# Performance work log

Hardware: AMD Instinct MI355X
Metric: run time of the kernel (lower is better)

## Reference

```python
import jax, jax.numpy as jnp
import numpy as np

DEPTH = 16      # env_depth: number of sequential beam-search steps
TEMP = 20.0     # softmax temperature (forward default temp=20)
NEG = -1e9      # -inf surrogate for dead beams (grad-safe)


def setup_inputs() -> dict:
    key = jax.random.key(0)
    ks = jax.random.split(key, 7)
    B, H, D = 256, 512, 64
    u = lambda k, s: jax.random.uniform(k, s, jnp.float32, -0.1, 0.1)
    return {
        "env": jax.random.normal(ks[0], (B, D), jnp.float32),
        "root_state": u(ks[1], (1, H)),
        "W_logits": u(ks[2], (H, D)),
        "b_logits": u(ks[3], (D,)),
        "W_hh": u(ks[4], (H, H)),
        "b_hh": u(ks[5], (H,)),
        "emb": u(ks[6], (D, H)),
        "beams": 128,
    }


def reference(env, root_state, W_logits, b_logits, W_hh, b_hh, emb, beams):
    B = env.shape[0]
    H = root_state.shape[1]
    D = W_logits.shape[1]

    # All beams start at the (shared, learned) root state; only beam 0 is live.
    states = jnp.broadcast_to(root_state[None, :, :], (B, beams, H))  # [B, K, H]
    scores = jnp.where(jnp.arange(beams) == 0, 0.0, NEG).astype(jnp.float32)
    scores = jnp.broadcast_to(scores[None, :], (B, beams))            # [B, K]
    hist = jnp.zeros((B, beams, DEPTH), jnp.int32)                    # chosen decisions

    def step(carry, t):
        states, scores, hist = carry
        # RNN router step: logits over decisions, temperature-scaled log-softmax
        logits = jnp.einsum('bkh,hd->bkd', states, W_logits) + b_logits  # [B,K,D]
        logp = jax.nn.log_softmax(logits / TEMP, axis=-1)
        # cumulative beam scores over all beams*decisions candidates
        cand = (scores[..., None] + logp).reshape(B, beams * D)
        top_scores, top_idx = jax.lax.top_k(cand, beams)                 # [B,K]
        beam_idx = top_idx // D                                          # parent beam
        dec = top_idx % D                                                # chosen decision
        # gather surviving beam state + history
        sel = jnp.take_along_axis(states, beam_idx[..., None], axis=1)   # [B,K,H]
        hist = jnp.take_along_axis(hist, beam_idx[..., None], axis=1)
        hist = hist.at[:, :, t].set(dec)
        # recurrent state update conditioned on chosen decision
        new_states = jnp.tanh(jnp.einsum('bkh,hg->bkg', sel, W_hh) + b_hh + emb[dec])
        return (new_states, top_scores, hist), None

    (states, scores, hist), _ = jax.lax.scan(step, (states, scores, hist), jnp.arange(DEPTH))
    return hist, scores
```

## Files before the change

### kernel.cpp

```cpp
#include <hip/hip_runtime.h>
#include <hip/hip_bf16.h>
#include <math.h>

#define NB    256
#define NK    128
#define NH    512
#define ND    64
#define NDEPTH 16
#define BKROWS (NB*NK)
#define TEMPD 20.0

typedef double d4 __attribute__((ext_vector_type(4)));

__global__ void k_init(const float* __restrict__ root, float* __restrict__ states,
                       double* __restrict__ scores, unsigned char* __restrict__ hist) {
    int idx = blockIdx.x * 256 + threadIdx.x;
    states[idx] = root[idx & (NH - 1)];
    if (idx < BKROWS) scores[idx] = ((idx & (NK - 1)) == 0) ? 0.0 : -1e9;
    if (idx < BKROWS * NDEPTH) hist[idx] = 0;
}

__global__ void __launch_bounds__(256, 4)
k_logits(const float* __restrict__ states,
         const float* __restrict__ Wl,
         const float* __restrict__ bl,
         const double* __restrict__ scores,
         double* __restrict__ cand)
{
    __shared__ double wl[16][64];
    __shared__ double stT[16][67];
    const int rowb = blockIdx.x * 64;
    const int t    = threadIdx.x;
    const int lane = t & 63;
    const int wv   = t >> 6;
    const int li   = lane & 15;
    const int kq   = lane >> 4;

    d4 acc[4];
    #pragma unroll
    for (int c = 0; c < 4; ++c) { acc[c][0]=0.0; acc[c][1]=0.0; acc[c][2]=0.0; acc[c][3]=0.0; }

    for (int kc = 0; kc < NH; kc += 16) {
        #pragma unroll
        for (int j = 0; j < 2; ++j) {
            int idx = j * 256 + t;
            int row = idx >> 5, cp = idx & 31;
            float2 v = *(const float2*)&Wl[(size_t)(kc + row) * ND + 2 * cp];
            double2 d; d.x = (double)v.x; d.y = (double)v.y;
            *(double2*)&wl[row][2 * cp] = d;
        }
        #pragma unroll
        for (int j = 0; j < 2; ++j) {
            int idx = j * 256 + t;
            int r = idx >> 3, cp = idx & 7;
            float2 v = *(const float2*)&states[(size_t)(rowb + r) * NH + kc + 2 * cp];
            stT[2 * cp][r]     = (double)v.x;
            stT[2 * cp + 1][r] = (double)v.y;
        }
        __syncthreads();

        #pragma unroll
        for (int ks = 0; ks < 4; ++ks) {
            int kk = 4 * ks + kq;
            double a  = stT[kk][wv * 16 + li];
            double b0 = wl[kk][     li];
            double b1 = wl[kk][16 + li];
            double b2 = wl[kk][32 + li];
            double b3 = wl[kk][48 + li];
            acc[0] = __builtin_amdgcn_mfma_f64_16x16x4f64(a, b0, acc[0], 0, 0, 0);
            acc[1] = __builtin_amdgcn_mfma_f64_16x16x4f64(a, b1, acc[1], 0, 0, 0);
            acc[2] = __builtin_amdgcn_mfma_f64_16x16x4f64(a, b2, acc[2], 0, 0, 0);
            acc[3] = __builtin_amdgcn_mfma_f64_16x16x4f64(a, b3, acc[3], 0, 0, 0);
        }
        __syncthreads();
    }

    const double bd0 = (double)bl[li];
    const double bd1 = (double)bl[16 + li];
    const double bd2 = (double)bl[32 + li];
    const double bd3 = (double)bl[48 + li];
    #pragma unroll
    for (int n = 0; n < 4; ++n) {
        int row = rowb + wv * 16 + kq + 4 * n;
        double x0 = (acc[0][n] + bd0) / TEMPD;
        double x1 = (acc[1][n] + bd1) / TEMPD;
        double x2 = (acc[2][n] + bd2) / TEMPD;
        double x3 = (acc[3][n] + bd3) / TEMPD;
        double m = fmax(fmax(x0, x1), fmax(x2, x3));
        #pragma unroll
        for (int off = 1; off <= 8; off <<= 1) m = fmax(m, __shfl_xor(m, off, 64));
        double e = exp(x0 - m) + exp(x1 - m) + exp(x2 - m) + exp(x3 - m);
        #pragma unroll
        for (int off = 1; off <= 8; off <<= 1) e += __shfl_xor(e, off, 64);
        double ls = log(e);
        double sc = scores[row];
        cand[(size_t)row * ND +      li] = sc + x0 - m - ls;
        cand[(size_t)row * ND + 16 + li] = sc + x1 - m - ls;
        cand[(size_t)row * ND + 32 + li] = sc + x2 - m - ls;
        cand[(size_t)row * ND + 48 + li] = sc + x3 - m - ls;
    }
}

__global__ void __launch_bounds__(256)
k_topk(const double* __restrict__ cand,
       double* __restrict__ scores,
       int* __restrict__ parent, int* __restrict__ decs,
       const unsigned char* __restrict__ hist_in,
       unsigned char* __restrict__ hist_out,
       int tstep)
{
    extern __shared__ double smem[];
    double* L  = smem;
    int*    sp = (int*)(smem + 128 * 65);
    int*    sd = sp + NK;

    const int b = blockIdx.x;
    const int t = threadIdx.x;
    const double* cb = cand + (size_t)b * (NK * ND);

    #pragma unroll
    for (int j = 0; j < 32; ++j) {
        int i = j * 256 + t;
        L[(i >> 6) * 65 + (i & 63)] = cb[i];
    }
    __syncthreads();

    if (t < 64) {
        const int lane = t;
        double mv = L[lane]; int mi = lane;
        for (int i = 1; i < 128; ++i) {
            double v = L[i * 65 + lane];
            if (v > mv) { mv = v; mi = i * 64 + lane; }
        }
        for (int it = 0; it < NK; ++it) {
            double m = mv; int idx = mi;
            #pragma unroll
            for (int off = 1; off <= 32; off <<= 1) {
                double m2 = __shfl_xor(m, off, 64);
                int    i2 = __shfl_xor(idx, off, 64);
                if (m2 > m || (m2 == m && i2 < idx)) { m = m2; idx = i2; }
            }
            const int wrow = idx >> 6, wcol = idx & 63;
            if (lane == 0) {
                scores[b * NK + it] = m;
                parent[b * NK + it] = wrow;
                decs  [b * NK + it] = wcol;
                sp[it] = wrow; sd[it] = wcol;
            }
            if (lane == wcol) L[wrow * 65 + wcol] = -INFINITY;
            double r0 = L[(2 * lane) * 65 + wcol];
            double r1 = L[(2 * lane + 1) * 65 + wcol];
            double rm; int ri;
            if (r1 > r0) { rm = r1; ri = (2 * lane + 1) * 64 + wcol; }
            else         { rm = r0; ri = (2 * lane) * 64 + wcol; }
            #pragma unroll
            for (int off = 1; off <= 32; off <<= 1) {
                double m2 = __shfl_xor(rm, off, 64);
                int    i2 = __shfl_xor(ri, off, 64);
                if (m2 > rm || (m2 == rm && i2 < ri)) { rm = m2; ri = i2; }
            }
            if (lane == wcol) { mv = rm; mi = ri; }
        }
    }
    __syncthreads();

    for (int i = t; i < NK * NDEPTH; i += 256) {
        int k = i >> 4, j = i & 15;
        hist_out[(b * NK + k) * NDEPTH + j] = (j == tstep) ? (unsigned char)sd[k]
                                            : hist_in[(b * NK + sp[k]) * NDEPTH + j];
    }
}

__global__ void __launch_bounds__(256, 4)
k_rnn(const float* __restrict__ states_in,
      const float* __restrict__ Whh,
      const float* __restrict__ bhh,
      const float* __restrict__ emb,
      const int* __restrict__ parent, const int* __restrict__ decs,
      float* __restrict__ states_out)
{
    __shared__ double wt[16][128];
    __shared__ double stT[16][67];
    __shared__ int sp[64], sd[64];

    const int rowb = blockIdx.x * 64;
    const int cbk  = blockIdx.y;
    const int colb = cbk * 128;
    const int t    = threadIdx.x;
    const int lane = t & 63;
    const int li   = lane & 15;
    const int kq   = lane >> 4;
    const int wv   = t >> 6;
    const int wm   = wv >> 1;
    const int wn   = wv & 1;

    if (t < 64) { sp[t] = parent[rowb + t]; sd[t] = decs[rowb + t]; }
    __syncthreads();

    int srow[2];
    #pragma unroll
    for (int j = 0; j < 2; ++j) {
        int r = (j * 256 + t) >> 3;
        srow[j] = ((rowb + r) >> 7) * NK + sp[r];
    }

    d4 acc[2][4];
    #pragma unroll
    for (int i = 0; i < 2; ++i)
        #pragma unroll
        for (int j = 0; j < 4; ++j) { acc[i][j][0]=0.0; acc[i][j][1]=0.0; acc[i][j][2]=0.0; acc[i][j][3]=0.0; }

    for (int kc = 0; kc < NH; kc += 16) {
        #pragma unroll
        for (int j = 0; j < 4; ++j) {
            int idx = j * 256 + t;
            int row = idx >> 6, cp = idx & 63;
            float2 v = *(const float2*)&Whh[(size_t)(kc + row) * NH + colb + 2 * cp];
            double2 d; d.x = (double)v.x; d.y = (double)v.y;
            *(double2*)&wt[row][2 * cp] = d;
        }
        #pragma unroll
        for (int j = 0; j < 2; ++j) {
            int idx = j * 256 + t;
            int r = idx >> 3, cp = idx & 7;
            float2 v = *(const float2*)&states_in[(size_t)srow[j] * NH + kc + 2 * cp];
            stT[2 * cp][r]     = (double)v.x;
            stT[2 * cp + 1][r] = (double)v.y;
        }
        __syncthreads();

        #pragma unroll
        for (int ks = 0; ks < 4; ++ks) {
            int kk = 4 * ks + kq;
            double a0 = stT[kk][wm * 32 + li];
            double a1 = stT[kk][wm * 32 + 16 + li];
            double b0 = wt[kk][wn * 64 +      li];
            double b1 = wt[kk][wn * 64 + 16 + li];
            double b2 = wt[kk][wn * 64 + 32 + li];
            double b3 = wt[kk][wn * 64 + 48 + li];
            acc[0][0] = __builtin_amdgcn_mfma_f64_16x16x4f64(a0, b0, acc[0][0], 0, 0, 0);
            acc[0][1] = __builtin_amdgcn_mfma_f64_16x16x4f64(a0, b1, acc[0][1], 0, 0, 0);
            acc[0][2] = __builtin_amdgcn_mfma_f64_16x16x4f64(a0, b2, acc[0][2], 0, 0, 0);
            acc[0][3] = __builtin_amdgcn_mfma_f64_16x16x4f64(a0, b3, acc[0][3], 0, 0, 0);
            acc[1][0] = __builtin_amdgcn_mfma_f64_16x16x4f64(a1, b0, acc[1][0], 0, 0, 0);
            acc[1][1] = __builtin_amdgcn_mfma_f64_16x16x4f64(a1, b1, acc[1][1], 0, 0, 0);
            acc[1][2] = __builtin_amdgcn_mfma_f64_16x16x4f64(a1, b2, acc[1][2], 0, 0, 0);
            acc[1][3] = __builtin_amdgcn_mfma_f64_16x16x4f64(a1, b3, acc[1][3], 0, 0, 0);
        }
        __syncthreads();
    }

    #pragma unroll
    for (int ct = 0; ct < 4; ++ct) {
        int col = colb + wn * 64 + ct * 16 + li;
        double bb = (double)bhh[col];
        #pragma unroll
        for (int rt = 0; rt < 2; ++rt) {
            #pragma unroll
            for (int n = 0; n < 4; ++n) {
                int rL = wm * 32 + rt * 16 + kq + 4 * n;
                double e = (double)emb[(size_t)sd[rL] * NH + col];
                double z = acc[rt][ct][n] + bb + e;
                states_out[(size_t)(rowb + rL) * NH + col] = (float)tanh(z);
            }
        }
    }
}

__global__ void k_final(const unsigned char* __restrict__ hist,
                        const double* __restrict__ scores,
                        float* __restrict__ out)
{
    int i = blockIdx.x * 256 + threadIdx.x;
    const int nh = BKROWS * NDEPTH;
    if (i < nh) out[i] = (float)hist[i];
    else if (i < nh + BKROWS) out[i] = (float)scores[i - nh];
}

extern "C" void kernel_launch(void* const* d_in, const int* in_sizes, int n_in,
                              void* d_out, int out_size, void* d_ws, size_t ws_size,
                              hipStream_t stream) {
    const float* root = (const float*)d_in[1];
    const float* Wl   = (const float*)d_in[2];
    const float* bl   = (const float*)d_in[3];
    const float* Whh  = (const float*)d_in[4];
    const float* bhh  = (const float*)d_in[5];
    const float* emb  = (const float*)d_in[6];

    char* ws = (char*)d_ws;
    double* cand         = (double*)(ws + 0);
    double* scores       = (double*)(ws + 16777216);
    float*  sA           = (float*)(ws + 17039360);
    float*  sB           = (float*)(ws + 84148224);
    int*    parent       = (int*)(ws + 151257088);
    int*    decs         = (int*)(ws + 151388160);
    unsigned char* hA    = (unsigned char*)(ws + 151519232);
    unsigned char* hB    = (unsigned char*)(ws + 152043520);

    k_init<<<65536, 256, 0, stream>>>(root, sA, scores, hA);

    float* scur = sA; float* snxt = sB;
    unsigned char* hcur = hA; unsigned char* hnxt = hB;
    for (int t = 0; t < NDEPTH; ++t) {
        k_logits<<<512, 256, 0, stream>>>(scur, Wl, bl, scores, cand);
        k_topk<<<256, 256, 67584, stream>>>(cand, scores, parent, decs, hcur, hnxt, t);
        k_rnn<<<dim3(512, 4), 256, 0, stream>>>(scur, Whh, bhh, emb, parent, decs, snxt);
        { float* tmp = scur; scur = snxt; snxt = tmp; }
        { unsigned char* tmp = hcur; hcur = hnxt; hnxt = tmp; }
    }

    k_final<<<2176, 256, 0, stream>>>(hcur, scores, (float*)d_out);
}
```

Before: 8.389 ms.

## Fuse logits/log-softmax GEMM with per-batch top-k selection kernel

Merges the logits GEMM plus log-softmax kernel with the top-k kernel. Each block now computes all 128 beam rows of one batch element and writes candidate scores straight into shared memory instead of a global cand buffer. This removes the 16MB global round trip and one launch per step. In exchange the logits GEMM runs on 256 blocks instead of 512, each with a larger shared footprint, which lowers parallelism and occupancy for the matmul phase.

```diff
diff --git a/kernel.cpp b/kernel.cpp
--- a/kernel.cpp
+++ b/kernel.cpp
@@ -20,25 +20,38 @@
     if (idx < BKROWS * NDEPTH) hist[idx] = 0;
 }
 
-__global__ void __launch_bounds__(256, 4)
-k_logits(const float* __restrict__ states,
-         const float* __restrict__ Wl,
-         const float* __restrict__ bl,
-         const double* __restrict__ scores,
-         double* __restrict__ cand)
+__global__ void __launch_bounds__(256)
+k_ltk(const float* __restrict__ states,
+      const float* __restrict__ Wl,
+      const float* __restrict__ bl,
+      double* __restrict__ scores,
+      int* __restrict__ parent, int* __restrict__ decs,
+      const unsigned char* __restrict__ hist_in,
+      unsigned char* __restrict__ hist_out,
+      int tstep)
 {
-    __shared__ double wl[16][64];
-    __shared__ double stT[16][67];
-    const int rowb = blockIdx.x * 64;
+    extern __shared__ char smem[];
+    double* L   = (double*)smem;
+    double* wl  = (double*)smem;
+    double* stT = (double*)(smem + 8192);
+    int* sp = (int*)(smem + 66560);
+    int* sd = sp + NK;
+
+    const int b    = blockIdx.x;
+    const int rowb = b * NK;
     const int t    = threadIdx.x;
     const int lane = t & 63;
     const int wv   = t >> 6;
     const int li   = lane & 15;
     const int kq   = lane >> 4;
 
-    d4 acc[4];
-    #pragma unroll
-    for (int c = 0; c < 4; ++c) { acc[c][0]=0.0; acc[c][1]=0.0; acc[c][2]=0.0; acc[c][3]=0.0; }
+    const int sr = t >> 3, scp = t & 7;
+
+    d4 acc[2][4];
+    #pragma unroll
+    for (int i = 0; i < 2; ++i)
+        #pragma unroll
+        for (int c = 0; c < 4; ++c) { acc[i][c][0]=0.0; acc[i][c][1]=0.0; acc[i][c][2]=0.0; acc[i][c][3]=0.0; }
 
     for (int kc = 0; kc < NH; kc += 16) {
         #pragma unroll
@@ -47,30 +60,34 @@
             int row = idx >> 5, cp = idx & 31;
             float2 v = *(const float2*)&Wl[(size_t)(kc + row) * ND + 2 * cp];
             double2 d; d.x = (double)v.x; d.y = (double)v.y;
-            *(double2*)&wl[row][2 * cp] = d;
-        }
-        #pragma unroll
-        for (int j = 0; j < 2; ++j) {
-            int idx = j * 256 + t;
-            int r = idx >> 3, cp = idx & 7;
-            float2 v = *(const float2*)&states[(size_t)(rowb + r) * NH + kc + 2 * cp];
-            stT[2 * cp][r]     = (double)v.x;
-            stT[2 * cp + 1][r] = (double)v.y;
+            *(double2*)&wl[row * 64 + 2 * cp] = d;
+        }
+        #pragma unroll
+        for (int j = 0; j < 4; ++j) {
+            int r = j * 32 + sr;
+            float2 v = *(const float2*)&states[(size_t)(rowb + r) * NH + kc + 2 * scp];
+            stT[(2 * scp) * 131 + r]     = (double)v.x;
+            stT[(2 * scp + 1) * 131 + r] = (double)v.y;
         }
         __syncthreads();
 
         #pragma unroll
         for (int ks = 0; ks < 4; ++ks) {
             int kk = 4 * ks + kq;
-            double a  = stT[kk][wv * 16 + li];
-            double b0 = wl[kk][     li];
-            double b1 = wl[kk][16 + li];
-            double b2 = wl[kk][32 + li];
-            double b3 = wl[kk][48 + li];
-            acc[0] = __builtin_amdgcn_mfma_f64_16x16x4f64(a, b0, acc[0], 0, 0, 0);
-            acc[1] = __builtin_amdgcn_mfma_f64_16x16x4f64(a, b1, acc[1], 0, 0, 0);
-            acc[2] = __builtin_amdgcn_mfma_f64_16x16x4f64(a, b2, acc[2], 0, 0, 0);
-            acc[3] = __builtin_amdgcn_mfma_f64_16x16x4f64(a, b3, acc[3], 0, 0, 0);
+            double a0 = stT[kk * 131 + wv * 32 +      li];
+            double a1 = stT[kk * 131 + wv * 32 + 16 + li];
+            double b0 = wl[kk * 64 +      li];
+            double b1 = wl[kk * 64 + 16 + li];
+            double b2 = wl[kk * 64 + 32 + li];
+            double b3 = wl[kk * 64 + 48 + li];
+            acc[0][0] = __builtin_amdgcn_mfma_f64_16x16x4f64(a0, b0, acc[0][0], 0, 0, 0);
+            acc[0][1] = __builtin_amdgcn_mfma_f64_16x16x4f64(a0, b1, acc[0][1], 0, 0, 0);
+            acc[0][2] = __builtin_amdgcn_mfma_f64_16x16x4f64(a0, b2, acc[0][2], 0, 0, 0);
+            acc[0][3] = __builtin_amdgcn_mfma_f64_16x16x4f64(a0, b3, acc[0][3], 0, 0, 0);
+            acc[1][0] = __builtin_amdgcn_mfma_f64_16x16x4f64(a1, b0, acc[1][0], 0, 0, 0);
+            acc[1][1] = __builtin_amdgcn_mfma_f64_16x16x4f64(a1, b1, acc[1][1], 0, 0, 0);
+            acc[1][2] = __builtin_amdgcn_mfma_f64_16x16x4f64(a1, b2, acc[1][2], 0, 0, 0);
+            acc[1][3] = __builtin_amdgcn_mfma_f64_16x16x4f64(a1, b3, acc[1][3], 0, 0, 0);
         }
         __syncthreads();
     }
@@ -80,57 +97,36 @@
     const double bd2 = (double)bl[32 + li];
     const double bd3 = (double)bl[48 + li];
     #pragma unroll
-    for (int n = 0; n < 4; ++n) {
-        int row = rowb + wv * 16 + kq + 4 * n;
-        double x0 = (acc[0][n] + bd0) / TEMPD;
-        double x1 = (acc[1][n] + bd1) / TEMPD;
-        double x2 = (acc[2][n] + bd2) / TEMPD;
-        double x3 = (acc[3][n] + bd3) / TEMPD;
-        double m = fmax(fmax(x0, x1), fmax(x2, x3));
-        #pragma unroll
-        for (int off = 1; off <= 8; off <<= 1) m = fmax(m, __shfl_xor(m, off, 64));
-        double e = exp(x0 - m) + exp(x1 - m) + exp(x2 - m) + exp(x3 - m);
-        #pragma unroll
-        for (int off = 1; off <= 8; off <<= 1) e += __shfl_xor(e, off, 64);
-        double ls = log(e);
-        double sc = scores[row];
-        cand[(size_t)row * ND +      li] = sc + x0 - m - ls;
-        cand[(size_t)row * ND + 16 + li] = sc + x1 - m - ls;
-        cand[(size_t)row * ND + 32 + li] = sc + x2 - m - ls;
-        cand[(size_t)row * ND + 48 + li] = sc + x3 - m - ls;
-    }
-}
-
-__global__ void __launch_bounds__(256)
-k_topk(const double* __restrict__ cand,
-       double* __restrict__ scores,
-       int* __restrict__ parent, int* __restrict__ decs,
-       const unsigned char* __restrict__ hist_in,
-       unsigned char* __restrict__ hist_out,
-       int tstep)
-{
-    extern __shared__ double smem[];
-    double* L  = smem;
-    int*    sp = (int*)(smem + 128 * 65);
-    int*    sd = sp + NK;
-
-    const int b = blockIdx.x;
-    const int t = threadIdx.x;
-    const double* cb = cand + (size_t)b * (NK * ND);
-
-    #pragma unroll
-    for (int j = 0; j < 32; ++j) {
-        int i = j * 256 + t;
-        L[(i >> 6) * 65 + (i & 63)] = cb[i];
+    for (int rt = 0; rt < 2; ++rt) {
+        #pragma unroll
+        for (int n = 0; n < 4; ++n) {
+            int rl = wv * 32 + rt * 16 + kq + 4 * n;
+            double x0 = (acc[rt][0][n] + bd0) / TEMPD;
+            double x1 = (acc[rt][1][n] + bd1) / TEMPD;
+            double x2 = (acc[rt][2][n] + bd2) / TEMPD;
+            double x3 = (acc[rt][3][n] + bd3) / TEMPD;
+            double m = fmax(fmax(x0, x1), fmax(x2, x3));
+            #pragma unroll
+            for (int off = 1; off <= 8; off <<= 1) m = fmax(m, __shfl_xor(m, off, 64));
+            double e = exp(x0 - m) + exp(x1 - m) + exp(x2 - m) + exp(x3 - m);
+            #pragma unroll
+            for (int off = 1; off <= 8; off <<= 1) e += __shfl_xor(e, off, 64);
+            double ls = log(e);
+            double sc = scores[rowb + rl];
+            L[rl * 65 +      li] = sc + x0 - m - ls;
+            L[rl * 65 + 16 + li] = sc + x1 - m - ls;
+            L[rl * 65 + 32 + li] = sc + x2 - m - ls;
+            L[rl * 65 + 48 + li] = sc + x3 - m - ls;
+        }
     }
     __syncthreads();
 
     if (t < 64) {
-        const int lane = t;
-        double mv = L[lane]; int mi = lane;
+        const int ln = t;
+        double mv = L[ln]; int mi = ln;
         for (int i = 1; i < 128; ++i) {
-            double v = L[i * 65 + lane];
-            if (v > mv) { mv = v; mi = i * 64 + lane; }
+            double v = L[i * 65 + ln];
+            if (v > mv) { mv = v; mi = i * 64 + ln; }
         }
         for (int it = 0; it < NK; ++it) {
             double m = mv; int idx = mi;
@@ -141,25 +137,25 @@
                 if (m2 > m || (m2 == m && i2 < idx)) { m = m2; idx = i2; }
             }
             const int wrow = idx >> 6, wcol = idx & 63;
-            if (lane == 0) {
+            if (ln == 0) {
                 scores[b * NK + it] = m;
                 parent[b * NK + it] = wrow;
                 decs  [b * NK + it] = wcol;
                 sp[it] = wrow; sd[it] = wcol;
             }
-            if (lane == wcol) L[wrow * 65 + wcol] = -INFINITY;
-            double r0 = L[(2 * lane) * 65 + wcol];
-            double r1 = L[(2 * lane + 1) * 65 + wcol];
+            if (ln == wcol) L[wrow * 65 + wcol] = -INFINITY;
+            double r0 = L[(2 * ln) * 65 + wcol];
+            double r1 = L[(2 * ln + 1) * 65 + wcol];
             double rm; int ri;
-            if (r1 > r0) { rm = r1; ri = (2 * lane + 1) * 64 + wcol; }
-            else         { rm = r0; ri = (2 * lane) * 64 + wcol; }
+            if (r1 > r0) { rm = r1; ri = (2 * ln + 1) * 64 + wcol; }
+            else         { rm = r0; ri = (2 * ln) * 64 + wcol; }
             #pragma unroll
             for (int off = 1; off <= 32; off <<= 1) {
                 double m2 = __shfl_xor(rm, off, 64);
                 int    i2 = __shfl_xor(ri, off, 64);
                 if (m2 > rm || (m2 == rm && i2 < ri)) { rm = m2; ri = i2; }
             }
-            if (lane == wcol) { mv = rm; mi = ri; }
+            if (ln == wcol) { mv = rm; mi = ri; }
         }
     }
     __syncthreads();
@@ -288,22 +284,20 @@
     const float* emb  = (const float*)d_in[6];
 
     char* ws = (char*)d_ws;
-    double* cand         = (double*)(ws + 0);
-    double* scores       = (double*)(ws + 16777216);
-    float*  sA           = (float*)(ws + 17039360);
-    float*  sB           = (float*)(ws + 84148224);
-    int*    parent       = (int*)(ws + 151257088);
-    int*    decs         = (int*)(ws + 151388160);
-    unsigned char* hA    = (unsigned char*)(ws + 151519232);
-    unsigned char* hB    = (unsigned char*)(ws + 152043520);
+    double* scores       = (double*)(ws + 0);
+    float*  sA           = (float*)(ws + 262144);
+    float*  sB           = (float*)(ws + 67371008);
+    int*    parent       = (int*)(ws + 134479872);
+    int*    decs         = (int*)(ws + 134610944);
+    unsigned char* hA    = (unsigned char*)(ws + 134742016);
+    unsigned char* hB    = (unsigned char*)(ws + 135266304);
 
     k_init<<<65536, 256, 0, stream>>>(root, sA, scores, hA);
 
     float* scur = sA; float* snxt = sB;
     unsigned char* hcur = hA; unsigned char* hnxt = hB;
     for (int t = 0; t < NDEPTH; ++t) {
-        k_logits<<<512, 256, 0, stream>>>(scur, Wl, bl, scores, cand);
-        k_topk<<<256, 256, 67584, stream>>>(cand, scores, parent, decs, hcur, hnxt, t);
+        k_ltk<<<256, 256, 67584, stream>>>(scur, Wl, bl, scores, parent, decs, hcur, hnxt, t);
         k_rnn<<<dim3(512, 4), 256, 0, stream>>>(scur, Whh, bhh, emb, parent, decs, snxt);
         { float* tmp = scur; scur = snxt; snxt = tmp; }
         { unsigned char* tmp = hcur; hcur = hnxt; hnxt = tmp; }
```

Result: slower. 8.642 ms (+3.0%).
